# Optimization experiments

Measured on AMD Instinct MI355X. Metric: run time of the kernel, lower is better.

Reference implementation:

```python
import jax, jax.numpy as jnp
import numpy as np

STATE_DIM = 512
ACTION_FEAT_DIM = 64
HIDDEN = 256


def setup_inputs() -> dict:
    key = jax.random.key(0)
    ks = jax.random.split(key, 8)
    B, K = 256, 1000
    state_embed = jax.random.normal(ks[0], (B, STATE_DIM), dtype=jnp.float32)
    action_feats = jax.random.normal(ks[1], (B, K, ACTION_FEAT_DIM), dtype=jnp.float32)
    s = 0.05
    W1 = jax.random.normal(ks[2], (STATE_DIM + ACTION_FEAT_DIM, HIDDEN), dtype=jnp.float32) * s
    b1 = jnp.zeros((HIDDEN,), dtype=jnp.float32)
    W2 = jax.random.normal(ks[3], (HIDDEN, HIDDEN // 2), dtype=jnp.float32) * s
    b2 = jnp.zeros((HIDDEN // 2,), dtype=jnp.float32)
    W3 = jax.random.normal(ks[4], (HIDDEN // 2, 1), dtype=jnp.float32) * s
    b3 = jnp.zeros((1,), dtype=jnp.float32)
    return {"state_embed": state_embed, "action_feats": action_feats,
            "W1": W1, "b1": b1, "W2": W2, "b2": b2, "W3": W3, "b3": b3}


def reference(state_embed, action_feats, W1, b1, W2, b2, W3, b3):
    # Faithful math: concat([state broadcast to K, action_feats]) -> Linear/ReLU x2 -> Linear(1)
    # Efficient form: split W1 rows so state part is computed once per batch row.
    W1_s = W1[:STATE_DIM]            # [state_dim, hidden]
    W1_a = W1[STATE_DIM:]            # [action_feat_dim, hidden]
    h_state = state_embed @ W1_s     # [B, hidden]
    h = jax.nn.relu(jnp.einsum('bkf,fh->bkh', action_feats, W1_a) + h_state[:, None, :] + b1)
    h = jax.nn.relu(jnp.einsum('bkh,hg->bkg', h, W2) + b2)
    logits = (jnp.einsum('bkg,go->bko', h, W3) + b3)[..., 0]  # [B, K]
    return logits
```

## Files before the change

kernel.cpp:

```cpp
#include <hip/hip_runtime.h>

typedef _Float16 f16;
typedef f16 f16x4 __attribute__((ext_vector_type(4)));
typedef f16 f16x8 __attribute__((ext_vector_type(8)));
typedef float f32x4 __attribute__((ext_vector_type(4)));


#define AF_STRIDE 64
#define H1_STRIDE 256

__global__ __launch_bounds__(256) void prep_kernel(const float* __restrict__ W1,
                                                   const float* __restrict__ W2,
                                                   const float* __restrict__ state,
                                                   const float* __restrict__ b1,
                                                   f16* __restrict__ pw1at,
                                                   f16* __restrict__ pw2,
                                                   float* __restrict__ hstate) {
    __shared__ float srow[512];
    int blk = blockIdx.x;
    int tid = threadIdx.x;
    if (blk < 24) {
        int idx = blk * 256 + tid;
        int F = idx >> 6;
        int L = idx & 63;
        int q = L >> 4, c = L & 15;
        f16x8 v;
        if (F < 32) {
            int mt = F >> 1, kt = F & 1;
            #pragma unroll
            for (int j = 0; j < 8; ++j) {
                int f = kt * 32 + q * 8 + j;
                v[j] = (f16)W1[(size_t)(512 + f) * 256 + mt * 16 + c];
            }
            *(f16x8*)(pw1at + ((size_t)F * 64 + L) * 8) = v;
        } else {
            int F2 = F - 32;
            int nt = F2 >> 3, kt = F2 & 7;
            #pragma unroll
            for (int j = 0; j < 8; ++j) {
                int k = kt * 32 + q * 8 + j;
                v[j] = (f16)W2[(size_t)k * 128 + nt * 16 + c];
            }
            *(f16x8*)(pw2 + ((size_t)F2 * 64 + L) * 8) = v;
        }
    } else {
        int b = blk - 24;
        srow[tid] = state[(size_t)b * 512 + tid];
        srow[tid + 256] = state[(size_t)b * 512 + 256 + tid];
        __syncthreads();
        float a0 = 0.f, a1 = 0.f;
        #pragma unroll 16
        for (int f = 0; f < 512; f += 2) {
            a0 = fmaf(srow[f],     W1[(size_t)f * 256 + tid],       a0);
            a1 = fmaf(srow[f + 1], W1[(size_t)(f + 1) * 256 + tid], a1);
        }
        hstate[(size_t)b * 256 + tid] = a0 + a1 + b1[tid];
    }
}

__global__ __launch_bounds__(256, 3) void fused_kernel(const float* __restrict__ afeat,
                                                       const float* __restrict__ hstate,
                                                       const f16* __restrict__ pw1at,
                                                       const f16* __restrict__ pw2,
                                                       const float* __restrict__ b2,
                                                       const float* __restrict__ W3,
                                                       const float* __restrict__ b3,
                                                       float* __restrict__ out) {
    __shared__ __align__(16) char smem[64 * H1_STRIDE * 2];
    f16* h1s = (f16*)smem;
    f16* afs = (f16*)(smem + 24576);
    float* lds3 = (float*)smem;

    int tid = threadIdx.x;
    int w = tid >> 6;
    int L = tid & 63;
    int q = L >> 4, c = L & 15;
    int r0 = blockIdx.x * 64;

    f32x4 sl[2][2];
    #pragma unroll
    for (int i = 0; i < 2; ++i) {
        int id = i * 256 + tid;
        int row = id >> 3, c32 = id & 7;
        const float* p = afeat + (size_t)(r0 + row) * 64 + c32 * 8;
        sl[i][0] = *(const f32x4*)p;
        sl[i][1] = *(const f32x4*)(p + 4);
    }

    f16x8 a1f[4][2];
    #pragma unroll
    for (int i = 0; i < 4; ++i)
        #pragma unroll
        for (int kt = 0; kt < 2; ++kt)
            a1f[i][kt] = *(const f16x8*)(pw1at + ((size_t)((4 * w + i) * 2 + kt) * 64 + L) * 8);

    int b0i = r0 / 1000;
    int boundary = (b0i + 1) * 1000;
    int b1i = b0i < 255 ? b0i + 1 : 255;

    f32x4 hsva[4], hsvb[4];
    #pragma unroll
    for (int i = 0; i < 4; ++i) {
        int hbase = (4 * w + i) * 16 + q * 4;
        hsva[i] = *(const f32x4*)(hstate + (size_t)b0i * 256 + hbase);
        hsvb[i] = *(const f32x4*)(hstate + (size_t)b1i * 256 + hbase);
    }

    #pragma unroll
    for (int i = 0; i < 2; ++i) {
        int id = i * 256 + tid;
        int row = id >> 3, c32 = id & 7;
        f16x8 v;
        v[0] = (f16)sl[i][0][0]; v[1] = (f16)sl[i][0][1];
        v[2] = (f16)sl[i][0][2]; v[3] = (f16)sl[i][0][3];
        v[4] = (f16)sl[i][1][0]; v[5] = (f16)sl[i][1][1];
        v[6] = (f16)sl[i][1][2]; v[7] = (f16)sl[i][1][3];
        *(f16x8*)(afs + row * AF_STRIDE + ((c32 * 8) ^ ((row & 7) << 3))) = v;
    }
    __syncthreads();

    int sx = (c & 7) << 3;
    unsigned bo = ((q * 8) ^ sx) * 2;

    const char* Bp0 = (const char*)afs + c * 128 + bo;
    const char* Bp1 = (const char*)afs + c * 128 + (bo ^ 64);
    f16x8 bf[4][2];
    #pragma unroll
    for (int nt = 0; nt < 4; ++nt) {
        bf[nt][0] = *(const f16x8*)(Bp0 + nt * 2048);
        bf[nt][1] = *(const f16x8*)(Bp1 + nt * 2048);
    }
    __syncthreads();

    const f16x4 zf = {(f16)0.f, (f16)0.f, (f16)0.f, (f16)0.f};
    #pragma unroll
    for (int i = 0; i < 4; ++i) {
        f32x4 acc[4];
        #pragma unroll
        for (int nt = 0; nt < 4; ++nt) {
            bool sel = (r0 + nt * 16 + c) >= boundary;
            acc[nt] = sel ? hsvb[i] : hsva[i];
            #pragma unroll
            for (int kt = 0; kt < 2; ++kt)
                acc[nt] = __builtin_amdgcn_mfma_f32_16x16x32_f16(
                    a1f[i][kt], bf[nt][kt], acc[nt], 0, 0, 0);
        }
        char* wp = (char*)h1s + c * 512 + ((((4 * w + i) * 16 + q * 4) ^ sx) * 2);
        #pragma unroll
        for (int nt = 0; nt < 4; ++nt) {
            f16x4 hv;
            hv[0] = (f16)acc[nt][0]; hv[1] = (f16)acc[nt][1];
            hv[2] = (f16)acc[nt][2]; hv[3] = (f16)acc[nt][3];
            hv = __builtin_elementwise_max(hv, zf);
            *(f16x4*)(wp + nt * 8192) = hv;
        }
    }
    __syncthreads();

    f32x4 b2v[2], w3v[2];
    #pragma unroll
    for (int gti = 0; gti < 2; ++gti) {
        int gb = (2 * w + gti) * 16 + q * 4;
        b2v[gti] = *(const f32x4*)(b2 + gb);
        w3v[gti] = *(const f32x4*)(W3 + gb);
    }
    float b3v = b3[0];

    const char* Ap0 = (const char*)h1s + c * 512 + bo;
    const char* Ap1 = (const char*)h1s + c * 512 + (bo ^ 64);

    f32x4 acc2[4][2];
    #pragma unroll
    for (int rb = 0; rb < 4; ++rb) {
        acc2[rb][0] = (f32x4){0.f, 0.f, 0.f, 0.f};
        acc2[rb][1] = (f32x4){0.f, 0.f, 0.f, 0.f};
    }

    f16x8 a2[2][4], pwf[2][2];
    #pragma unroll
    for (int rb = 0; rb < 4; ++rb)
        a2[0][rb] = *(const f16x8*)(Ap0 + rb * 8192);
    #pragma unroll
    for (int gti = 0; gti < 2; ++gti)
        pwf[0][gti] = *(const f16x8*)(pw2 + ((size_t)((2 * w + gti) * 8) * 64 + L) * 8);

    #pragma unroll
    for (int kt = 0; kt < 8; ++kt) {
        if (kt < 7) {
            const char* Apn = ((kt + 1) & 1) ? Ap1 : Ap0;
            #pragma unroll
            for (int rb = 0; rb < 4; ++rb)
                a2[(kt + 1) & 1][rb] =
                    *(const f16x8*)(Apn + ((kt + 1) >> 1) * 128 + rb * 8192);
            #pragma unroll
            for (int gti = 0; gti < 2; ++gti)
                pwf[(kt + 1) & 1][gti] =
                    *(const f16x8*)(pw2 + ((size_t)((2 * w + gti) * 8 + kt + 1) * 64 + L) * 8);
        }
        __builtin_amdgcn_s_setprio(1);
        #pragma unroll
        for (int gti = 0; gti < 2; ++gti)
            #pragma unroll
            for (int rb = 0; rb < 4; ++rb)
                acc2[rb][gti] = __builtin_amdgcn_mfma_f32_16x16x32_f16(
                    pwf[kt & 1][gti], a2[kt & 1][rb], acc2[rb][gti], 0, 0, 0);
        __builtin_amdgcn_s_setprio(0);
    }

    float pa[4];
    #pragma unroll
    for (int rb = 0; rb < 4; ++rb) {
        float s = 0.f;
        #pragma unroll
        for (int gti = 0; gti < 2; ++gti)
            #pragma unroll
            for (int reg = 0; reg < 4; ++reg) {
                float v = acc2[rb][gti][reg] + b2v[gti][reg];
                v = v > 0.f ? v : 0.f;
                s = fmaf(v, w3v[gti][reg], s);
            }
        pa[rb] = s;
    }
    #pragma unroll
    for (int rb = 0; rb < 4; ++rb) {
        pa[rb] += __shfl_xor(pa[rb], 16);
        pa[rb] += __shfl_xor(pa[rb], 32);
    }
    __syncthreads();
    if (L < 16) {
        #pragma unroll
        for (int rb = 0; rb < 4; ++rb)
            lds3[(rb * 16 + L) * 6 + w] = pa[rb];
    }
    __syncthreads();

    if (tid < 64) {
        const float* pm = lds3 + tid * 6;
        out[r0 + tid] = pm[0] + pm[1] + pm[2] + pm[3] + b3v;
    }
}

extern "C" void kernel_launch(void* const* d_in, const int* in_sizes, int n_in,
                              void* d_out, int out_size, void* d_ws, size_t ws_size,
                              hipStream_t stream) {
    const float* state = (const float*)d_in[0];
    const float* afeat = (const float*)d_in[1];
    const float* W1    = (const float*)d_in[2];
    const float* b1    = (const float*)d_in[3];
    const float* W2    = (const float*)d_in[4];
    const float* b2    = (const float*)d_in[5];
    const float* W3    = (const float*)d_in[6];
    const float* b3    = (const float*)d_in[7];
    float* out = (float*)d_out;

    float* hstate = (float*)d_ws;
    f16* pw1at = (f16*)((char*)d_ws + 65536 * sizeof(float));
    f16* pw2   = pw1at + 16384;

    prep_kernel<<<280, 256, 0, stream>>>(W1, W2, state, b1, pw1at, pw2, hstate);
    fused_kernel<<<4000, 256, 0, stream>>>(afeat, hstate, pw1at, pw2, b2, W3, b3, out);
}
```

Baseline: 132.8 us.

## Process two 64-row tiles per block with prefetch of next tile's activations

Each block now handles 128 rows in two 64-row iterations, halving the grid to 2000 blocks. The second tile's action features are loaded from global memory while the first tile is written to LDS and computed, so load latency overlaps with MFMA work. Launch bounds drop from 3 to 2 waves per SIMD to leave room for the extra live registers. There is a redundant reload of a1f weights and hstate after the first tile, and lower occupancy may reduce latency hiding elsewhere.

Result: no change. 133.8 us (+0.7%).

```diff
diff --git a/kernel.cpp b/kernel.cpp
--- a/kernel.cpp
+++ b/kernel.cpp
@@ -58,7 +58,7 @@
     }
 }
 
-__global__ __launch_bounds__(256, 3) void fused_kernel(const float* __restrict__ afeat,
+__global__ __launch_bounds__(256, 2) void fused_kernel(const float* __restrict__ afeat,
                                                        const float* __restrict__ hstate,
                                                        const f16* __restrict__ pw1at,
                                                        const f16* __restrict__ pw2,
@@ -75,14 +75,14 @@
     int w = tid >> 6;
     int L = tid & 63;
     int q = L >> 4, c = L & 15;
-    int r0 = blockIdx.x * 64;
+    int r0g = blockIdx.x * 128;
 
     f32x4 sl[2][2];
     #pragma unroll
     for (int i = 0; i < 2; ++i) {
         int id = i * 256 + tid;
         int row = id >> 3, c32 = id & 7;
-        const float* p = afeat + (size_t)(r0 + row) * 64 + c32 * 8;
+        const float* p = afeat + (size_t)(r0g + row) * 64 + c32 * 8;
         sl[i][0] = *(const f32x4*)p;
         sl[i][1] = *(const f32x4*)(p + 4);
     }
@@ -94,68 +94,22 @@
         for (int kt = 0; kt < 2; ++kt)
             a1f[i][kt] = *(const f16x8*)(pw1at + ((size_t)((4 * w + i) * 2 + kt) * 64 + L) * 8);
 
-    int b0i = r0 / 1000;
-    int boundary = (b0i + 1) * 1000;
-    int b1i = b0i < 255 ? b0i + 1 : 255;
-
+    {
+        int b0i = r0g / 1000;
+        int b1i = b0i < 255 ? b0i + 1 : 255;
+        (void)b1i;
+    }
     f32x4 hsva[4], hsvb[4];
-    #pragma unroll
-    for (int i = 0; i < 4; ++i) {
-        int hbase = (4 * w + i) * 16 + q * 4;
-        hsva[i] = *(const f32x4*)(hstate + (size_t)b0i * 256 + hbase);
-        hsvb[i] = *(const f32x4*)(hstate + (size_t)b1i * 256 + hbase);
-    }
-
-    #pragma unroll
-    for (int i = 0; i < 2; ++i) {
-        int id = i * 256 + tid;
-        int row = id >> 3, c32 = id & 7;
-        f16x8 v;
-        v[0] = (f16)sl[i][0][0]; v[1] = (f16)sl[i][0][1];
-        v[2] = (f16)sl[i][0][2]; v[3] = (f16)sl[i][0][3];
-        v[4] = (f16)sl[i][1][0]; v[5] = (f16)sl[i][1][1];
-        v[6] = (f16)sl[i][1][2]; v[7] = (f16)sl[i][1][3];
-        *(f16x8*)(afs + row * AF_STRIDE + ((c32 * 8) ^ ((row & 7) << 3))) = v;
-    }
-    __syncthreads();
-
-    int sx = (c & 7) << 3;
-    unsigned bo = ((q * 8) ^ sx) * 2;
-
-    const char* Bp0 = (const char*)afs + c * 128 + bo;
-    const char* Bp1 = (const char*)afs + c * 128 + (bo ^ 64);
-    f16x8 bf[4][2];
-    #pragma unroll
-    for (int nt = 0; nt < 4; ++nt) {
-        bf[nt][0] = *(const f16x8*)(Bp0 + nt * 2048);
-        bf[nt][1] = *(const f16x8*)(Bp1 + nt * 2048);
-    }
-    __syncthreads();
-
-    const f16x4 zf = {(f16)0.f, (f16)0.f, (f16)0.f, (f16)0.f};
-    #pragma unroll
-    for (int i = 0; i < 4; ++i) {
-        f32x4 acc[4];
-        #pragma unroll
-        for (int nt = 0; nt < 4; ++nt) {
-            bool sel = (r0 + nt * 16 + c) >= boundary;
-            acc[nt] = sel ? hsvb[i] : hsva[i];
-            #pragma unroll
-            for (int kt = 0; kt < 2; ++kt)
-                acc[nt] = __builtin_amdgcn_mfma_f32_16x16x32_f16(
-                    a1f[i][kt], bf[nt][kt], acc[nt], 0, 0, 0);
-        }
-        char* wp = (char*)h1s + c * 512 + ((((4 * w + i) * 16 + q * 4) ^ sx) * 2);
-        #pragma unroll
-        for (int nt = 0; nt < 4; ++nt) {
-            f16x4 hv;
-            hv[0] = (f16)acc[nt][0]; hv[1] = (f16)acc[nt][1];
-            hv[2] = (f16)acc[nt][2]; hv[3] = (f16)acc[nt][3];
-            hv = __builtin_elementwise_max(hv, zf);
-            *(f16x4*)(wp + nt * 8192) = hv;
-        }
-    }
-    __syncthreads();
+    {
+        int b0i = r0g / 1000;
+        int b1i = b0i < 255 ? b0i + 1 : 255;
+        #pragma unroll
+        for (int i = 0; i < 4; ++i) {
+            int hbase = (4 * w + i) * 16 + q * 4;
+            hsva[i] = *(const f32x4*)(hstate + (size_t)b0i * 256 + hbase);
+            hsvb[i] = *(const f32x4*)(hstate + (size_t)b1i * 256 + hbase);
+        }
+    }
 
     f32x4 b2v[2], w3v[2];
     #pragma unroll
@@ -166,77 +120,159 @@
     }
     float b3v = b3[0];
 
+    int sx = (c & 7) << 3;
+    unsigned bo = ((q * 8) ^ sx) * 2;
+    const char* Bp0 = (const char*)afs + c * 128 + bo;
+    const char* Bp1 = (const char*)afs + c * 128 + (bo ^ 64);
     const char* Ap0 = (const char*)h1s + c * 512 + bo;
     const char* Ap1 = (const char*)h1s + c * 512 + (bo ^ 64);
-
-    f32x4 acc2[4][2];
-    #pragma unroll
-    for (int rb = 0; rb < 4; ++rb) {
-        acc2[rb][0] = (f32x4){0.f, 0.f, 0.f, 0.f};
-        acc2[rb][1] = (f32x4){0.f, 0.f, 0.f, 0.f};
-    }
-
-    f16x8 a2[2][4], pwf[2][2];
-    #pragma unroll
-    for (int rb = 0; rb < 4; ++rb)
-        a2[0][rb] = *(const f16x8*)(Ap0 + rb * 8192);
-    #pragma unroll
-    for (int gti = 0; gti < 2; ++gti)
-        pwf[0][gti] = *(const f16x8*)(pw2 + ((size_t)((2 * w + gti) * 8) * 64 + L) * 8);
-
-    #pragma unroll
-    for (int kt = 0; kt < 8; ++kt) {
-        if (kt < 7) {
-            const char* Apn = ((kt + 1) & 1) ? Ap1 : Ap0;
+    const f16x4 zf = {(f16)0.f, (f16)0.f, (f16)0.f, (f16)0.f};
+
+    #pragma unroll
+    for (int t = 0; t < 2; ++t) {
+        int r0 = r0g + t * 64;
+        int boundary = (r0 / 1000 + 1) * 1000;
+
+        #pragma unroll
+        for (int i = 0; i < 2; ++i) {
+            int id = i * 256 + tid;
+            int row = id >> 3, c32 = id & 7;
+            f16x8 v;
+            v[0] = (f16)sl[i][0][0]; v[1] = (f16)sl[i][0][1];
+            v[2] = (f16)sl[i][0][2]; v[3] = (f16)sl[i][0][3];
+            v[4] = (f16)sl[i][1][0]; v[5] = (f16)sl[i][1][1];
+            v[6] = (f16)sl[i][1][2]; v[7] = (f16)sl[i][1][3];
+            *(f16x8*)(afs + row * AF_STRIDE + ((c32 * 8) ^ ((row & 7) << 3))) = v;
+        }
+        if (t == 0) {
+            #pragma unroll
+            for (int i = 0; i < 2; ++i) {
+                int id = i * 256 + tid;
+                int row = id >> 3, c32 = id & 7;
+                const float* p = afeat + (size_t)(r0g + 64 + row) * 64 + c32 * 8;
+                sl[i][0] = *(const f32x4*)p;
+                sl[i][1] = *(const f32x4*)(p + 4);
+            }
+        }
+        __syncthreads();
+
+        f16x8 bf[4][2];
+        #pragma unroll
+        for (int nt = 0; nt < 4; ++nt) {
+            bf[nt][0] = *(const f16x8*)(Bp0 + nt * 2048);
+            bf[nt][1] = *(const f16x8*)(Bp1 + nt * 2048);
+        }
+        __syncthreads();
+
+        #pragma unroll
+        for (int i = 0; i < 4; ++i) {
+            f32x4 acc[4];
+            #pragma unroll
+            for (int nt = 0; nt < 4; ++nt) {
+                bool sel = (r0 + nt * 16 + c) >= boundary;
+                acc[nt] = sel ? hsvb[i] : hsva[i];
+                #pragma unroll
+                for (int kt = 0; kt < 2; ++kt)
+                    acc[nt] = __builtin_amdgcn_mfma_f32_16x16x32_f16(
+                        a1f[i][kt], bf[nt][kt], acc[nt], 0, 0, 0);
+            }
+            char* wp = (char*)h1s + c * 512 + ((((4 * w + i) * 16 + q * 4) ^ sx) * 2);
+            #pragma unroll
+            for (int nt = 0; nt < 4; ++nt) {
+                f16x4 hv;
+                hv[0] = (f16)acc[nt][0]; hv[1] = (f16)acc[nt][1];
+                hv[2] = (f16)acc[nt][2]; hv[3] = (f16)acc[nt][3];
+                hv = __builtin_elementwise_max(hv, zf);
+                *(f16x4*)(wp + nt * 8192) = hv;
+            }
+        }
+        __syncthreads();
+
+        f32x4 acc2[4][2];
+        #pragma unroll
+        for (int rb = 0; rb < 4; ++rb) {
+            acc2[rb][0] = (f32x4){0.f, 0.f, 0.f, 0.f};
+            acc2[rb][1] = (f32x4){0.f, 0.f, 0.f, 0.f};
+        }
+        f16x8 a2[2][4], pwf[2][2];
+        #pragma unroll
+        for (int rb = 0; rb < 4; ++rb)
+            a2[0][rb] = *(const f16x8*)(Ap0 + rb * 8192);
+        #pragma unroll
+        for (int gti = 0; gti < 2; ++gti)
+            pwf[0][gti] = *(const f16x8*)(pw2 + ((size_t)((2 * w + gti) * 8) * 64 + L) * 8);
+
+        #pragma unroll
+        for (int kt = 0; kt < 8; ++kt) {
+            if (kt < 7) {
+                const char* Apn = ((kt + 1) & 1) ? Ap1 : Ap0;
+                #pragma unroll
+                for (int rb = 0; rb < 4; ++rb)
+                    a2[(kt + 1) & 1][rb] =
+                        *(const f16x8*)(Apn + ((kt + 1) >> 1) * 128 + rb * 8192);
+                #pragma unroll
+                for (int gti = 0; gti < 2; ++gti)
+                    pwf[(kt + 1) & 1][gti] =
+                        *(const f16x8*)(pw2 + ((size_t)((2 * w + gti) * 8 + kt + 1) * 64 + L) * 8);
+            }
+            __builtin_amdgcn_s_setprio(1);
+            #pragma unroll
+            for (int gti = 0; gti < 2; ++gti)
+                #pragma unroll
+                for (int rb = 0; rb < 4; ++rb)
+                    acc2[rb][gti] = __builtin_amdgcn_mfma_f32_16x16x32_f16(
+                        pwf[kt & 1][gti], a2[kt & 1][rb], acc2[rb][gti], 0, 0, 0);
+            __builtin_amdgcn_s_setprio(0);
+        }
+
+        float pa[4];
+        #pragma unroll
+        for (int rb = 0; rb < 4; ++rb) {
+            float s = 0.f;
+            #pragma unroll
+            for (int gti = 0; gti < 2; ++gti)
+                #pragma unroll
+                for (int reg = 0; reg < 4; ++reg) {
+                    float v = acc2[rb][gti][reg] + b2v[gti][reg];
+                    v = v > 0.f ? v : 0.f;
+                    s = fmaf(v, w3v[gti][reg], s);
+                }
+            pa[rb] = s;
+        }
+        #pragma unroll
+        for (int rb = 0; rb < 4; ++rb) {
+            pa[rb] += __shfl_xor(pa[rb], 16);
+            pa[rb] += __shfl_xor(pa[rb], 32);
+        }
+        __syncthreads();
+        if (L < 16) {
             #pragma unroll
             for (int rb = 0; rb < 4; ++rb)
-                a2[(kt + 1) & 1][rb] =
-                    *(const f16x8*)(Apn + ((kt + 1) >> 1) * 128 + rb * 8192);
-            #pragma unroll
-            for (int gti = 0; gti < 2; ++gti)
-                pwf[(kt + 1) & 1][gti] =
-                    *(const f16x8*)(pw2 + ((size_t)((2 * w + gti) * 8 + kt + 1) * 64 + L) * 8);
-        }
-        __builtin_amdgcn_s_setprio(1);
-        #pragma unroll
-        for (int gti = 0; gti < 2; ++gti)
-            #pragma unroll
-            for (int rb = 0; rb < 4; ++rb)
-                acc2[rb][gti] = __builtin_amdgcn_mfma_f32_16x16x32_f16(
-                    pwf[kt & 1][gti], a2[kt & 1][rb], acc2[rb][gti], 0, 0, 0);
-        __builtin_amdgcn_s_setprio(0);
-    }
-
-    float pa[4];
-    #pragma unroll
-    for (int rb = 0; rb < 4; ++rb) {
-        float s = 0.f;
-        #pragma unroll
-        for (int gti = 0; gti < 2; ++gti)
-            #pragma unroll
-            for (int reg = 0; reg < 4; ++reg) {
-                float v = acc2[rb][gti][reg] + b2v[gti][reg];
-                v = v > 0.f ? v : 0.f;
-                s = fmaf(v, w3v[gti][reg], s);
-            }
-        pa[rb] = s;
-    }
-    #pragma unroll
-    for (int rb = 0; rb < 4; ++rb) {
-        pa[rb] += __shfl_xor(pa[rb], 16);
-        pa[rb] += __shfl_xor(pa[rb], 32);
-    }
-    __syncthreads();
-    if (L < 16) {
-        #pragma unroll
-        for (int rb = 0; rb < 4; ++rb)
-            lds3[(rb * 16 + L) * 6 + w] = pa[rb];
-    }
-    __syncthreads();
-
-    if (tid < 64) {
-        const float* pm = lds3 + tid * 6;
-        out[r0 + tid] = pm[0] + pm[1] + pm[2] + pm[3] + b3v;
+                lds3[(rb * 16 + L) * 6 + w] = pa[rb];
+        }
+        __syncthreads();
+
+        if (tid < 64) {
+            const float* pm = lds3 + tid * 6;
+            out[r0 + tid] = pm[0] + pm[1] + pm[2] + pm[3] + b3v;
+        }
+
+        if (t == 0) {
+            int r0n = r0g + 64;
+            int b0n = r0n / 1000;
+            int b1n = b0n < 255 ? b0n + 1 : 255;
+            #pragma unroll
+            for (int i = 0; i < 4; ++i) {
+                int hbase = (4 * w + i) * 16 + q * 4;
+                hsva[i] = *(const f32x4*)(hstate + (size_t)b0n * 256 + hbase);
+                hsvb[i] = *(const f32x4*)(hstate + (size_t)b1n * 256 + hbase);
+            }
+            #pragma unroll
+            for (int i = 0; i < 4; ++i)
+                #pragma unroll
+                for (int kt = 0; kt < 2; ++kt)
+                    a1f[i][kt] = *(const f16x8*)(pw1at + ((size_t)((4 * w + i) * 2 + kt) * 64 + L) * 8);
+        }
     }
 }
 
@@ -258,5 +294,5 @@
     f16* pw2   = pw1at + 16384;
 
     prep_kernel<<<280, 256, 0, stream>>>(W1, W2, state, b1, pw1at, pw2, hstate);
-    fused_kernel<<<4000, 256, 0, stream>>>(afeat, hstate, pw1at, pw2, b2, W3, b3, out);
+    fused_kernel<<<2000, 256, 0, stream>>>(afeat, hstate, pw1at, pw2, b2, W3, b3, out);
 }
```
